# Kernel optimization log

Hardware: AMD Instinct MI355X
Metric: run time of the kernel (lower is better)

## Reference

```python
import jax, jax.numpy as jnp
import numpy as np

B, S, DM = 2, 2048, 1024
H, DH = 16, 64
SCALE = jnp.sqrt(jnp.float32(DH))  # dot_scale = sqrt(dim_head)


def setup_inputs() -> dict:
    key = jax.random.key(0)
    ks = jax.random.split(key, 9)
    std = 1.0 / np.sqrt(DM)
    x = jax.random.normal(ks[0], (B, S, DM), dtype=jnp.float32)
    Wq = jax.random.uniform(ks[1], (DM, DM), jnp.float32, -std, std)
    bq = jax.random.uniform(ks[2], (DM,), jnp.float32, -std, std)
    Wk = jax.random.uniform(ks[3], (DM, DM), jnp.float32, -std, std)
    bk = jax.random.uniform(ks[4], (DM,), jnp.float32, -std, std)
    Wv = jax.random.uniform(ks[5], (DM, DM), jnp.float32, -std, std)
    bv = jax.random.uniform(ks[6], (DM,), jnp.float32, -std, std)
    Wo = jax.random.uniform(ks[7], (DM, DM), jnp.float32, -std, std)
    bo = jax.random.uniform(ks[8], (DM,), jnp.float32, -std, std)
    # causal mask: 1 = masked (future positions), broadcast over batch
    causal = jnp.triu(jnp.ones((S, S), dtype=jnp.int32), k=1)
    attention_mask = jnp.broadcast_to(causal, (B, S, S))
    return {"x": x, "Wq": Wq, "bq": bq, "Wk": Wk, "bk": bk,
            "Wv": Wv, "bv": bv, "Wo": Wo, "bo": bo,
            "attention_mask": attention_mask}


def reference(x, Wq, bq, Wk, bk, Wv, bv, Wo, bo, attention_mask):
    # Linear layers (torch nn.Linear: y = x @ W^T + b)
    q = (x @ Wq.T + bq).reshape(B, S, H, DH).transpose(0, 2, 1, 3)  # (B,H,S,DH)
    k = (x @ Wk.T + bk).reshape(B, S, H, DH).transpose(0, 2, 1, 3)  # (B,H,S,DH)
    v = (x @ Wv.T + bv).reshape(B, S, H, DH).transpose(0, 2, 1, 3)  # (B,H,S,DH)
    # scores: (B,H,S,S), then mask==1 -> -inf, softmax over last dim
    scores = jnp.einsum('bhsd,bhtd->bhst', q, k) / SCALE
    mask = attention_mask[:, None, :, :]  # (B,1,S,S)
    scores = jnp.where(mask == 1, -jnp.inf, scores)
    attn = jax.nn.softmax(scores, axis=-1)
    # dropout is identity in eval mode
    ctx = jnp.einsum('bhst,bhtd->bshd', attn, v).reshape(B, S, H * DH)
    return ctx @ Wo.T + bo
```

## Files before the change

### kernel.cpp

```cpp
#include <hip/hip_runtime.h>
#include <stdint.h>

typedef unsigned short u16;
typedef __attribute__((ext_vector_type(8))) short bf16x8;
typedef __attribute__((ext_vector_type(4))) float f32x4;

#define BATCH 2
#define S_LEN 2048
#define DMODEL 1024
#define NH 16
#define DHEAD 64
#define MTOT 4096
#define QSCALE 0.18033688011112042f

#define GL2LDS(g, l) \
  __builtin_amdgcn_global_load_lds((const __attribute__((address_space(1))) void*)(g), \
                                   (__attribute__((address_space(3))) void*)(l), 16, 0, 0)

__device__ __forceinline__ u16 f2bf(float x) {
  union { float f; uint32_t u; } v; v.f = x;
  uint32_t r = v.u + 0x7fffu + ((v.u >> 16) & 1u);
  return (u16)(r >> 16);
}
__device__ __forceinline__ u16 f2bf_fast(float x) {
  union { float f; uint32_t u; } v; v.f = x;
  return (u16)((v.u + 0x8000u) >> 16);
}

struct CvtArgs {
  const float* src[5];
  u16* dst[5];
};

__global__ __launch_bounds__(256) void cvt_all(CvtArgs a) {
  int bx = blockIdx.x;
  int region, off;
  if (bx < 4096) { region = 0; off = bx; }
  else { region = 1 + ((bx - 4096) >> 10); off = (bx - 4096) & 1023; }
  const float* s = a.src[region];
  u16* d = a.dst[region];
  int i = (off * 256 + threadIdx.x) * 4;
  float4 v = *(const float4*)(s + i);
  uint2 pk;
  pk.x = (uint32_t)f2bf(v.x) | ((uint32_t)f2bf(v.y) << 16);
  pk.y = (uint32_t)f2bf(v.z) | ((uint32_t)f2bf(v.w) << 16);
  *(uint2*)(d + i) = pk;
}

__device__ __forceinline__ void gemm_body(const u16* __restrict__ A,
                                          const u16* __restrict__ W,
                                          const float* __restrict__ bias,
                                          void* __restrict__ out,
                                          int mode, float scale,
                                          int m0, int n0) {
  __shared__ u16 As[2][128 * 32];
  __shared__ u16 Bs[2][128 * 32];
  const int tid = threadIdx.x;
  const int wave = tid >> 6, lane = tid & 63;
  const int wm = (wave >> 1) * 64, wn = (wave & 1) * 64;
  const int quad = lane >> 4, l15 = lane & 15;

  const int row0 = tid >> 2, g0 = ((tid & 3) ^ (row0 & 3)) * 8;
  const int row1 = (tid + 256) >> 2, g1 = ((tid & 3) ^ (row1 & 3)) * 8;
  const int lb0 = wave * 512;
  const int lb1 = 2048 + wave * 512;
  const int xk = (quad ^ (l15 & 3)) * 8;

  f32x4 acc[4][4] = {};

#define GSTAGE(kt_, pb)                                                     \
  do {                                                                      \
    GL2LDS(A + (size_t)(m0 + row0) * DMODEL + (kt_) + g0, &As[pb][0] + lb0);\
    GL2LDS(A + (size_t)(m0 + row1) * DMODEL + (kt_) + g1, &As[pb][0] + lb1);\
    GL2LDS(W + (size_t)(n0 + row0) * DMODEL + (kt_) + g0, &Bs[pb][0] + lb0);\
    GL2LDS(W + (size_t)(n0 + row1) * DMODEL + (kt_) + g1, &Bs[pb][0] + lb1);\
  } while (0)

  GSTAGE(0, 0);
  for (int t = 0; t < 32; ++t) {
    const int p = t & 1;
    __syncthreads();
    if (t < 31) GSTAGE((t + 1) * 32, p ^ 1);
    bf16x8 af[4], bfr[4];
#pragma unroll
    for (int bi = 0; bi < 4; ++bi)
      af[bi] = *(const bf16x8*)(&As[p][(wm + bi * 16 + l15) * 32 + xk]);
#pragma unroll
    for (int bj = 0; bj < 4; ++bj)
      bfr[bj] = *(const bf16x8*)(&Bs[p][(wn + bj * 16 + l15) * 32 + xk]);
#pragma unroll
    for (int bi = 0; bi < 4; ++bi)
#pragma unroll
      for (int bj = 0; bj < 4; ++bj)
        acc[bi][bj] = __builtin_amdgcn_mfma_f32_16x16x32_bf16(af[bi], bfr[bj], acc[bi][bj], 0, 0, 0);
  }
#undef GSTAGE

#pragma unroll
  for (int bi = 0; bi < 4; ++bi) {
#pragma unroll
    for (int bj = 0; bj < 4; ++bj) {
      int n = n0 + wn + bj * 16 + l15;
      float bval = bias[n];
#pragma unroll
      for (int r = 0; r < 4; ++r) {
        int m = m0 + wm + bi * 16 + quad * 4 + r;
        float v = (acc[bi][bj][r] + bval) * scale;
        u16 bvu = f2bf(v);
        int b = m >> 11, s = m & 2047;
        int h = n >> 6, d = n & 63;
        size_t bh = (size_t)(b * NH + h);
        if (mode == 1)
          ((u16*)out)[(bh * S_LEN + s) * DHEAD + d] = bvu;
        else
          ((u16*)out)[((bh * 256 + (s >> 3)) * 64 + d) * 8 + (s & 7)] = bvu;
      }
    }
  }
}

struct QKVArgs {
  const u16* w[3];
  const float* b[3];
  u16* o[3];
};

__global__ __launch_bounds__(256, 3) void qkv_gemm(const u16* __restrict__ xb, QKVArgs a) {
  int s = blockIdx.x;
  int xcd = s & 7, idx = s >> 3;
  int xx = idx & 3, yy = (idx >> 2) & 7, z = idx >> 5;
  int nt = (xcd & 1) * 4 + xx;
  int mt = (xcd >> 1) * 8 + yy;
  int mode = (z == 2) ? 2 : 1;
  float scale = (z == 0) ? QSCALE : 1.0f;
  gemm_body(xb, a.w[z], a.b[z], a.o[z], mode, scale, mt * 128, nt * 128);
}

__global__ __launch_bounds__(256, 3) void out_gemm(const u16* __restrict__ A,
                                                   const u16* __restrict__ W,
                                                   const float* __restrict__ bias,
                                                   float* __restrict__ out) {
  int sb = blockIdx.x;
  int xcd = sb & 7, idx = sb >> 3;
  int xx = idx & 7, yy = idx >> 3;
  const int n0 = ((xcd & 1) * 8 + xx) * 64;
  const int m0 = ((xcd >> 1) * 8 + yy) * 128;

  __shared__ u16 As[2][128 * 32];
  __shared__ u16 Bs[2][64 * 32];
  const int tid = threadIdx.x;
  const int wave = tid >> 6, lane = tid & 63;
  const int wm = (wave >> 1) * 64, wn = (wave & 1) * 32;
  const int quad = lane >> 4, l15 = lane & 15;

  const int row0 = tid >> 2, g0 = ((tid & 3) ^ (row0 & 3)) * 8;
  const int row1 = (tid + 256) >> 2, g1 = ((tid & 3) ^ (row1 & 3)) * 8;
  const int lb0 = wave * 512;
  const int lb1 = 2048 + wave * 512;
  const int xk = (quad ^ (l15 & 3)) * 8;

  f32x4 acc[4][2] = {};

#define OSTAGE(kt_, pb)                                                     \
  do {                                                                      \
    GL2LDS(A + (size_t)(m0 + row0) * DMODEL + (kt_) + g0, &As[pb][0] + lb0);\
    GL2LDS(A + (size_t)(m0 + row1) * DMODEL + (kt_) + g1, &As[pb][0] + lb1);\
    GL2LDS(W + (size_t)(n0 + row0) * DMODEL + (kt_) + g0, &Bs[pb][0] + lb0);\
  } while (0)

  OSTAGE(0, 0);
  for (int t = 0; t < 32; ++t) {
    const int p = t & 1;
    __syncthreads();
    if (t < 31) OSTAGE((t + 1) * 32, p ^ 1);
    bf16x8 af[4], bfr[2];
#pragma unroll
    for (int bi = 0; bi < 4; ++bi)
      af[bi] = *(const bf16x8*)(&As[p][(wm + bi * 16 + l15) * 32 + xk]);
#pragma unroll
    for (int bj = 0; bj < 2; ++bj)
      bfr[bj] = *(const bf16x8*)(&Bs[p][(wn + bj * 16 + l15) * 32 + xk]);
#pragma unroll
    for (int bi = 0; bi < 4; ++bi)
#pragma unroll
      for (int bj = 0; bj < 2; ++bj)
        acc[bi][bj] = __builtin_amdgcn_mfma_f32_16x16x32_bf16(af[bi], bfr[bj], acc[bi][bj], 0, 0, 0);
  }
#undef OSTAGE

#pragma unroll
  for (int bi = 0; bi < 4; ++bi) {
#pragma unroll
    for (int bj = 0; bj < 2; ++bj) {
      int n = n0 + wn + bj * 16 + l15;
      float bval = bias[n];
#pragma unroll
      for (int r = 0; r < 4; ++r) {
        int m = m0 + wm + bi * 16 + quad * 4 + r;
        out[(size_t)m * DMODEL + n] = acc[bi][bj][r] + bval;
      }
    }
  }
}

__global__ __launch_bounds__(256, 4) void attn(const u16* __restrict__ Q,
                                               const u16* __restrict__ Kg,
                                               const u16* __restrict__ Vt8,
                                               u16* __restrict__ ctx) {
  __shared__ u16 Kd[2][64 * 64];
  __shared__ u16 Vd[2][64 * 64];
  __shared__ u16 Ps[64 * 64];
  const int tid = threadIdx.x;
  const int g = blockIdx.x >> 5;
  const int bh = blockIdx.x & 31;
  const int gv = g & 7;
  int qt = (g & 8) ? (15 - gv) : gv;
  if (g & 16) qt += 16;
  const int wave = tid >> 6, lane = tid & 63;
  const int quad = lane >> 4, l15 = lane & 15;
  const size_t base = (size_t)bh * S_LEN * DHEAD;
  const int b = bh >> 4, h = bh & 15;
  const int xk7 = l15 & 7;

#define STAGE(kt_, pb)                                                                   \
  do {                                                                                   \
    _Pragma("unroll")                                                                    \
    for (int i_ = 0; i_ < 2; ++i_) {                                                     \
      int c_ = tid + 256 * i_;                                                           \
      int row_ = c_ >> 3, g_ = ((c_ & 7) ^ (row_ & 7)) * 8;                              \
      GL2LDS(Kg + base + (size_t)((kt_) * 64 + row_) * 64 + g_,                          \
             &Kd[pb][0] + i_ * 2048 + wave * 512);                                       \
      GL2LDS(Vt8 + base + (size_t)((kt_) * 512 + c_) * 8,                                \
             &Vd[pb][0] + i_ * 2048 + wave * 512);                                       \
    }                                                                                    \
  } while (0)

  const int qrow = qt * 64 + wave * 16 + l15;
  bf16x8 qf0 = *(const bf16x8*)(Q + base + (size_t)qrow * DHEAD + quad * 8);
  bf16x8 qf1 = *(const bf16x8*)(Q + base + (size_t)qrow * DHEAD + 32 + quad * 8);

  float l_part[4] = {0.f, 0.f, 0.f, 0.f};
  f32x4 o[4] = {};

  STAGE(0, 0);

  for (int kt = 0; kt <= qt; ++kt) {
    const int p = kt & 1;
    __syncthreads();
    if (kt < qt) STAGE(kt + 1, p ^ 1);

    const bool diag = (kt == qt);
    f32x4 s_acc[4];
#pragma unroll
    for (int bj = 0; bj < 4; ++bj) {
      if (diag && bj > wave) {
        s_acc[bj] = f32x4{-1e30f, -1e30f, -1e30f, -1e30f};
        continue;
      }
      const int krow = (bj * 16 + l15) * 64;
      bf16x8 kf0 = *(const bf16x8*)(&Kd[p][krow + ((quad ^ xk7) * 8)]);
      bf16x8 kf1 = *(const bf16x8*)(&Kd[p][krow + (((quad + 4) ^ xk7) * 8)]);
      f32x4 t = {0.f, 0.f, 0.f, 0.f};
      t = __builtin_amdgcn_mfma_f32_16x16x32_bf16(qf0, kf0, t, 0, 0, 0);
      t = __builtin_amdgcn_mfma_f32_16x16x32_bf16(qf1, kf1, t, 0, 0, 0);
      s_acc[bj] = t;
    }

    if (diag) {
#pragma unroll
      for (int bj = 0; bj < 4; ++bj) {
        int kg = kt * 64 + bj * 16 + l15;
#pragma unroll
        for (int r = 0; r < 4; ++r) {
          int qg = qt * 64 + wave * 16 + quad * 4 + r;
          if (kg > qg) s_acc[bj][r] = -1e30f;
        }
      }
    }

#pragma unroll
    for (int bj = 0; bj < 4; ++bj) {
#pragma unroll
      for (int r = 0; r < 4; ++r) {
        float pv = exp2f(s_acc[bj][r]);
        l_part[r] += pv;
        int row = wave * 16 + quad * 4 + r;
        int ch = (bj * 2 + (l15 >> 3)) ^ (row & 7);
        Ps[row * 64 + ch * 8 + (l15 & 7)] = f2bf_fast(pv);
      }
    }

    {
      const int row2 = wave * 16 + l15;
#pragma unroll
      for (int kk = 0; kk < 2; ++kk) {
        bf16x8 pf = *(const bf16x8*)(&Ps[row2 * 64 + (((kk << 2) + quad) ^ xk7) * 8]);
#pragma unroll
        for (int dj = 0; dj < 4; ++dj) {
          bf16x8 vf = *(const bf16x8*)(&Vd[p][((kk * 4 + quad) * 64 + dj * 16 + l15) * 8]);
          o[dj] = __builtin_amdgcn_mfma_f32_16x16x32_bf16(pf, vf, o[dj], 0, 0, 0);
        }
      }
    }
  }

#pragma unroll
  for (int r = 0; r < 4; ++r) {
    float s = l_part[r];
    s += __shfl_xor(s, 1, 64);
    s += __shfl_xor(s, 2, 64);
    s += __shfl_xor(s, 4, 64);
    s += __shfl_xor(s, 8, 64);
    float inv = 1.0f / s;
    int srow = qt * 64 + wave * 16 + quad * 4 + r;
    size_t rowbase = ((size_t)b * S_LEN + srow) * DMODEL + h * DHEAD;
#pragma unroll
    for (int dj = 0; dj < 4; ++dj)
      ctx[rowbase + dj * 16 + l15] = f2bf(o[dj][r] * inv);
  }
#undef STAGE
}

extern "C" void kernel_launch(void* const* d_in, const int* in_sizes, int n_in,
                              void* d_out, int out_size, void* d_ws, size_t ws_size,
                              hipStream_t stream) {
  const float* x  = (const float*)d_in[0];
  const float* Wq = (const float*)d_in[1];
  const float* bq = (const float*)d_in[2];
  const float* Wk = (const float*)d_in[3];
  const float* bk = (const float*)d_in[4];
  const float* Wv = (const float*)d_in[5];
  const float* bv = (const float*)d_in[6];
  const float* Wo = (const float*)d_in[7];
  const float* bo = (const float*)d_in[8];
  float* out = (float*)d_out;

  char* ws = (char*)d_ws;
  const size_t MB = 1u << 20;
  u16* xb   = (u16*)(ws + 0);
  u16* ctxb = xb;
  u16* wqb  = (u16*)(ws + 8 * MB);
  u16* wkb  = (u16*)(ws + 10 * MB);
  u16* wvb  = (u16*)(ws + 12 * MB);
  u16* wob  = (u16*)(ws + 14 * MB);
  u16* qb   = (u16*)(ws + 16 * MB);
  u16* kb   = (u16*)(ws + 24 * MB);
  u16* vtb  = (u16*)(ws + 32 * MB);

  CvtArgs c;
  c.src[0] = x;  c.dst[0] = xb;
  c.src[1] = Wq; c.dst[1] = wqb;
  c.src[2] = Wk; c.dst[2] = wkb;
  c.src[3] = Wv; c.dst[3] = wvb;
  c.src[4] = Wo; c.dst[4] = wob;
  cvt_all<<<4096 + 4 * 1024, 256, 0, stream>>>(c);

  QKVArgs a;
  a.w[0] = wqb; a.w[1] = wkb; a.w[2] = wvb;
  a.b[0] = bq;  a.b[1] = bk;  a.b[2] = bv;
  a.o[0] = qb;  a.o[1] = kb;  a.o[2] = vtb;
  qkv_gemm<<<768, 256, 0, stream>>>(xb, a);

  attn<<<1024, 256, 0, stream>>>(qb, kb, vtb, ctxb);

  out_gemm<<<512, 256, 0, stream>>>(ctxb, wob, bo, out);
}
```

Baseline: 208.6 us.

## Use 128-row Q tiles with 32x32 MFMA, register-resident P, and split-K combine

```diff
diff --git a/kernel.cpp b/kernel.cpp
--- a/kernel.cpp
+++ b/kernel.cpp
@@ -4,6 +4,8 @@
 typedef unsigned short u16;
 typedef __attribute__((ext_vector_type(8))) short bf16x8;
 typedef __attribute__((ext_vector_type(4))) float f32x4;
+typedef __attribute__((ext_vector_type(16))) float f32x16;
+typedef __attribute__((ext_vector_type(4))) uint32_t u32x4;
 
 #define BATCH 2
 #define S_LEN 2048
@@ -22,9 +24,11 @@
   uint32_t r = v.u + 0x7fffu + ((v.u >> 16) & 1u);
   return (u16)(r >> 16);
 }
-__device__ __forceinline__ u16 f2bf_fast(float x) {
-  union { float f; uint32_t u; } v; v.f = x;
-  return (u16)((v.u + 0x8000u) >> 16);
+
+__device__ __forceinline__ uint32_t cvtpk_bf16(float lo, float hi) {
+  uint32_t r;
+  asm("v_cvt_pk_bf16_f32 %0, %1, %2" : "=v"(r) : "v"(lo), "v"(hi));
+  return r;
 }
 
 struct CvtArgs {
@@ -206,21 +210,29 @@
 __global__ __launch_bounds__(256, 4) void attn(const u16* __restrict__ Q,
                                                const u16* __restrict__ Kg,
                                                const u16* __restrict__ Vt8,
-                                               u16* __restrict__ ctx) {
+                                               u16* __restrict__ ctx,
+                                               float* __restrict__ part_o,
+                                               float* __restrict__ part_l) {
   __shared__ u16 Kd[2][64 * 64];
   __shared__ u16 Vd[2][64 * 64];
-  __shared__ u16 Ps[64 * 64];
   const int tid = threadIdx.x;
-  const int g = blockIdx.x >> 5;
+  const int q3 = blockIdx.x >> 8;
+  const int t = (blockIdx.x >> 5) & 7;
   const int bh = blockIdx.x & 31;
-  const int gv = g & 7;
-  int qt = (g & 8) ? (15 - gv) : gv;
-  if (g & 16) qt += 16;
   const int wave = tid >> 6, lane = tid & 63;
-  const int quad = lane >> 4, l15 = lane & 15;
+  const int l31 = lane & 31, hi = lane >> 5;
   const size_t base = (size_t)bh * S_LEN * DHEAD;
   const int b = bh >> 4, h = bh & 15;
-  const int xk7 = l15 & 7;
+
+  int qs, k0, k1, slot = 0;
+  if (q3 == 0) { qs = t; k0 = 0; k1 = 2 * t + 1; }
+  else {
+    qs = 15 - t;
+    int half = qs + 1;
+    if (q3 == 1) { k0 = 0; k1 = half - 1; }
+    else         { k0 = half; k1 = 2 * qs + 1; }
+    slot = ((qs - 8) * 2 + (q3 - 1)) * 32 + bh;
+  }
 
 #define STAGE(kt_, pb)                                                                   \
   do {                                                                                   \
@@ -235,90 +247,126 @@
     }                                                                                    \
   } while (0)
 
-  const int qrow = qt * 64 + wave * 16 + l15;
-  bf16x8 qf0 = *(const bf16x8*)(Q + base + (size_t)qrow * DHEAD + quad * 8);
-  bf16x8 qf1 = *(const bf16x8*)(Q + base + (size_t)qrow * DHEAD + 32 + quad * 8);
-
-  float l_part[4] = {0.f, 0.f, 0.f, 0.f};
-  f32x4 o[4] = {};
-
-  STAGE(0, 0);
-
-  for (int kt = 0; kt <= qt; ++kt) {
-    const int p = kt & 1;
+  const int q0 = qs * 128 + wave * 32;
+  bf16x8 qf[4];
+#pragma unroll
+  for (int s = 0; s < 4; ++s)
+    qf[s] = *(const bf16x8*)(Q + base + (size_t)(q0 + l31) * DHEAD + s * 16 + hi * 8);
+
+  f32x16 o0 = {}, o1 = {};
+  float lp = 0.f;
+
+  STAGE(k0, 0);
+  for (int kt = k0; kt <= k1; ++kt) {
+    const int p = (kt - k0) & 1;
     __syncthreads();
-    if (kt < qt) STAGE(kt + 1, p ^ 1);
-
-    const bool diag = (kt == qt);
-    f32x4 s_acc[4];
-#pragma unroll
-    for (int bj = 0; bj < 4; ++bj) {
-      if (diag && bj > wave) {
-        s_acc[bj] = f32x4{-1e30f, -1e30f, -1e30f, -1e30f};
-        continue;
-      }
-      const int krow = (bj * 16 + l15) * 64;
-      bf16x8 kf0 = *(const bf16x8*)(&Kd[p][krow + ((quad ^ xk7) * 8)]);
-      bf16x8 kf1 = *(const bf16x8*)(&Kd[p][krow + (((quad + 4) ^ xk7) * 8)]);
-      f32x4 t = {0.f, 0.f, 0.f, 0.f};
-      t = __builtin_amdgcn_mfma_f32_16x16x32_bf16(qf0, kf0, t, 0, 0, 0);
-      t = __builtin_amdgcn_mfma_f32_16x16x32_bf16(qf1, kf1, t, 0, 0, 0);
-      s_acc[bj] = t;
+    if (kt < k1) STAGE(kt + 1, p ^ 1);
+
+    const int kb0 = kt * 64;
+    if (kb0 <= q0 + 31) {
+      const u16* Kt = &Kd[p][0];
+      const u16* Vt = &Vd[p][0];
+      f32x16 sa0 = {}, sa1 = {};
+#pragma unroll
+      for (int s = 0; s < 4; ++s) {
+        bf16x8 kf0 = *(const bf16x8*)(&Kt[l31 * 64 + (((s * 2 + hi) ^ (l31 & 7)) * 8)]);
+        sa0 = __builtin_amdgcn_mfma_f32_32x32x16_bf16(kf0, qf[s], sa0, 0, 0, 0);
+      }
+#pragma unroll
+      for (int s = 0; s < 4; ++s) {
+        bf16x8 kf1 = *(const bf16x8*)(&Kt[(32 + l31) * 64 + (((s * 2 + hi) ^ (l31 & 7)) * 8)]);
+        sa1 = __builtin_amdgcn_mfma_f32_32x32x16_bf16(kf1, qf[s], sa1, 0, 0, 0);
+      }
+      if (kb0 + 63 > q0) {
+        const int qg = q0 + l31;
+#pragma unroll
+        for (int r = 0; r < 16; ++r) {
+          int kg = kb0 + (r & 3) + 4 * hi + 8 * (r >> 2);
+          if (kg > qg) sa0[r] = -1e30f;
+          if (kg + 32 > qg) sa1[r] = -1e30f;
+        }
+      }
+#pragma unroll
+      for (int r = 0; r < 16; ++r) { sa0[r] = exp2f(sa0[r]); lp += sa0[r]; }
+#pragma unroll
+      for (int r = 0; r < 16; ++r) { sa1[r] = exp2f(sa1[r]); lp += sa1[r]; }
+      uint32_t P2[2][8];
+#pragma unroll
+      for (int m = 0; m < 8; ++m) {
+        P2[0][m] = cvtpk_bf16(sa0[2 * m], sa0[2 * m + 1]);
+        P2[1][m] = cvtpk_bf16(sa1[2 * m], sa1[2 * m + 1]);
+      }
+#pragma unroll
+      for (int n = 0; n < 4; ++n) {
+        const int kb = n >> 1, mb = 4 * (n & 1);
+        uint32_t A0 = P2[kb][mb], A0p = P2[kb][mb + 1];
+        uint32_t A1 = P2[kb][mb + 2], A1p = P2[kb][mb + 3];
+        uint32_t X0  = (uint32_t)__shfl_xor((int)A0, 32, 64);
+        uint32_t X0p = (uint32_t)__shfl_xor((int)A0p, 32, 64);
+        uint32_t X1  = (uint32_t)__shfl_xor((int)A1, 32, 64);
+        uint32_t X1p = (uint32_t)__shfl_xor((int)A1p, 32, 64);
+        u32x4 pw;
+        pw.x = hi ? X1 : A0;
+        pw.y = hi ? X1p : A0p;
+        pw.z = hi ? A1 : X0;
+        pw.w = hi ? A1p : X0p;
+        bf16x8 pfv = __builtin_bit_cast(bf16x8, pw);
+        bf16x8 vf0 = *(const bf16x8*)(&Vt[((2 * n + hi) * 64 + l31) * 8]);
+        bf16x8 vf1 = *(const bf16x8*)(&Vt[((2 * n + hi) * 64 + 32 + l31) * 8]);
+        o0 = __builtin_amdgcn_mfma_f32_32x32x16_bf16(pfv, vf0, o0, 0, 0, 0);
+        o1 = __builtin_amdgcn_mfma_f32_32x32x16_bf16(pfv, vf1, o1, 0, 0, 0);
+      }
     }
-
-    if (diag) {
-#pragma unroll
-      for (int bj = 0; bj < 4; ++bj) {
-        int kg = kt * 64 + bj * 16 + l15;
-#pragma unroll
-        for (int r = 0; r < 4; ++r) {
-          int qg = qt * 64 + wave * 16 + quad * 4 + r;
-          if (kg > qg) s_acc[bj][r] = -1e30f;
-        }
-      }
+  }
+
+  lp += __shfl_xor(lp, 32, 64);
+
+  if (q3 == 0) {
+    float inv = 1.0f / lp;
+#pragma unroll
+    for (int r = 0; r < 16; ++r) {
+      int rl = (r & 3) + 4 * hi + 8 * (r >> 2);
+      float invr = __shfl(inv, rl, 64);
+      int q = q0 + rl;
+      size_t rb = ((size_t)b * S_LEN + q) * DMODEL + h * DHEAD;
+      ctx[rb + l31] = f2bf(o0[r] * invr);
+      ctx[rb + 32 + l31] = f2bf(o1[r] * invr);
     }
-
-#pragma unroll
-    for (int bj = 0; bj < 4; ++bj) {
-#pragma unroll
-      for (int r = 0; r < 4; ++r) {
-        float pv = exp2f(s_acc[bj][r]);
-        l_part[r] += pv;
-        int row = wave * 16 + quad * 4 + r;
-        int ch = (bj * 2 + (l15 >> 3)) ^ (row & 7);
-        Ps[row * 64 + ch * 8 + (l15 & 7)] = f2bf_fast(pv);
-      }
+  } else {
+    float* po = part_o + (size_t)slot * 8192 + (size_t)wave * 32 * 64;
+#pragma unroll
+    for (int r = 0; r < 16; ++r) {
+      int rl = (r & 3) + 4 * hi + 8 * (r >> 2);
+      po[rl * 64 + l31] = o0[r];
+      po[rl * 64 + 32 + l31] = o1[r];
     }
-
-    {
-      const int row2 = wave * 16 + l15;
-#pragma unroll
-      for (int kk = 0; kk < 2; ++kk) {
-        bf16x8 pf = *(const bf16x8*)(&Ps[row2 * 64 + (((kk << 2) + quad) ^ xk7) * 8]);
-#pragma unroll
-        for (int dj = 0; dj < 4; ++dj) {
-          bf16x8 vf = *(const bf16x8*)(&Vd[p][((kk * 4 + quad) * 64 + dj * 16 + l15) * 8]);
-          o[dj] = __builtin_amdgcn_mfma_f32_16x16x32_bf16(pf, vf, o[dj], 0, 0, 0);
-        }
-      }
-    }
-  }
-
-#pragma unroll
-  for (int r = 0; r < 4; ++r) {
-    float s = l_part[r];
-    s += __shfl_xor(s, 1, 64);
-    s += __shfl_xor(s, 2, 64);
-    s += __shfl_xor(s, 4, 64);
-    s += __shfl_xor(s, 8, 64);
-    float inv = 1.0f / s;
-    int srow = qt * 64 + wave * 16 + quad * 4 + r;
-    size_t rowbase = ((size_t)b * S_LEN + srow) * DMODEL + h * DHEAD;
-#pragma unroll
-    for (int dj = 0; dj < 4; ++dj)
-      ctx[rowbase + dj * 16 + l15] = f2bf(o[dj][r] * inv);
+    if (hi == 0) part_l[(size_t)slot * 128 + wave * 32 + l31] = lp;
   }
 #undef STAGE
+}
+
+__global__ __launch_bounds__(256) void combine(const float* __restrict__ part_o,
+                                               const float* __restrict__ part_l,
+                                               u16* __restrict__ ctx) {
+  const int pidx = blockIdx.x;
+  const int qs8 = pidx >> 5, bh = pidx & 31;
+  const int qs = 8 + qs8;
+  const int b = bh >> 4, h = bh & 15;
+  const float* poA = part_o + (size_t)((qs8 * 2 + 0) * 32 + bh) * 8192;
+  const float* poB = part_o + (size_t)((qs8 * 2 + 1) * 32 + bh) * 8192;
+  const float* plA = part_l + (size_t)((qs8 * 2 + 0) * 32 + bh) * 128;
+  const float* plB = part_l + (size_t)((qs8 * 2 + 1) * 32 + bh) * 128;
+  for (int i = threadIdx.x * 4; i < 8192; i += 1024) {
+    int row = i >> 6, col = i & 63;
+    float4 oa = *(const float4*)(poA + i);
+    float4 ob = *(const float4*)(poB + i);
+    float inv = 1.0f / (plA[row] + plB[row]);
+    uint2 pk;
+    pk.x = (uint32_t)f2bf((oa.x + ob.x) * inv) | ((uint32_t)f2bf((oa.y + ob.y) * inv) << 16);
+    pk.y = (uint32_t)f2bf((oa.z + ob.z) * inv) | ((uint32_t)f2bf((oa.w + ob.w) * inv) << 16);
+    int srow = qs * 128 + row;
+    *(uint2*)(ctx + ((size_t)b * S_LEN + srow) * DMODEL + h * DHEAD + col) = pk;
+  }
 }
 
 extern "C" void kernel_launch(void* const* d_in, const int* in_sizes, int n_in,
@@ -346,6 +394,8 @@
   u16* qb   = (u16*)(ws + 16 * MB);
   u16* kb   = (u16*)(ws + 24 * MB);
   u16* vtb  = (u16*)(ws + 32 * MB);
+  float* part_o = (float*)d_out;
+  float* part_l = (float*)(ws + 8 * MB);
 
   CvtArgs c;
   c.src[0] = x;  c.dst[0] = xb;
@@ -361,7 +411,9 @@
   a.o[0] = qb;  a.o[1] = kb;  a.o[2] = vtb;
   qkv_gemm<<<768, 256, 0, stream>>>(xb, a);
 
-  attn<<<1024, 256, 0, stream>>>(qb, kb, vtb, ctxb);
+  attn<<<768, 256, 0, stream>>>(qb, kb, vtb, ctxb, part_o, part_l);
+
+  combine<<<256, 256, 0, stream>>>(part_o, part_l, ctxb);
 
   out_gemm<<<512, 256, 0, stream>>>(ctxb, wob, bo, out);
 }
```

Result: no change. 208.6 us (-0.0%).
